# Optimization experiments

Measured on AMD Instinct MI355X. Metric: run time of the kernel, lower is better.

The kernel has to match this reference:

```python
import jax, jax.numpy as jnp
from jax import lax
import numpy as np

B, N, NPOINT, NSAMPLE, RADIUS = 8, 16384, 1024, 32, 0.4
C_IN = 64


def fps(xyz, npoint):
    """Furthest point sampling. xyz: (B, N, 3) -> (B, npoint) int32 indices.
    Matches the CUDA kernel: start from index 0, iteratively pick argmax of
    the running min-distance to the selected set."""
    Bb, Nn, _ = xyz.shape

    def step(carry, _):
        min_d, last = carry
        p = jnp.take_along_axis(xyz, last[:, None, None], axis=1)  # (B,1,3)
        d = jnp.sum((xyz - p) ** 2, axis=-1)                       # (B,N)
        min_d = jnp.minimum(min_d, d)
        nxt = jnp.argmax(min_d, axis=1).astype(jnp.int32)
        return (min_d, nxt), nxt

    idx0 = jnp.zeros((Bb,), jnp.int32)
    min_d0 = jnp.full((Bb, Nn), jnp.inf, xyz.dtype)
    _, rest = lax.scan(step, (min_d0, idx0), None, length=npoint - 1)  # (npoint-1, B)
    return jnp.transpose(jnp.concatenate([idx0[None, :], rest], axis=0))  # (B, npoint)


def ball_query(xyz, new_xyz, radius, nsample):
    """xyz: (B,N,3), new_xyz: (B,P,3) -> (B,P,nsample) int32 indices.
    First nsample in-radius indices (ascending), short balls padded with the
    first found index (the centroid itself is always in-radius)."""
    Nn = xyz.shape[1]
    d2 = jnp.sum((new_xyz[:, :, None, :] - xyz[:, None, :, :]) ** 2, axis=-1)  # (B,P,N)
    ar = jnp.arange(Nn, dtype=jnp.int32)
    key = jnp.where(d2 <= radius * radius, ar, Nn)  # out-of-ball -> sentinel N
    neg_top, _ = lax.top_k(-key, nsample)           # nsample smallest keys
    gidx = -neg_top                                  # (B,P,nsample)
    return jnp.where(gidx == Nn, gidx[..., :1], gidx)


def setup_inputs() -> dict:
    key = jax.random.key(0)
    ks = jax.random.split(key, 8)
    return {
        "xyz": jax.random.normal(ks[0], (B, N, 3), jnp.float32),
        "features": jax.random.normal(ks[1], (B, C_IN, N), jnp.float32),
        "W1": jax.random.normal(ks[2], (64, 3 + C_IN), jnp.float32) * 0.05,
        "b1": jax.random.normal(ks[3], (64,), jnp.float32) * 0.05,
        "W2": jax.random.normal(ks[4], (64, 64), jnp.float32) * 0.05,
        "b2": jax.random.normal(ks[5], (64,), jnp.float32) * 0.05,
        "W3": jax.random.normal(ks[6], (128, 64), jnp.float32) * 0.05,
        "b3": jax.random.normal(ks[7], (128,), jnp.float32) * 0.05,
    }


def reference(xyz, features, W1, b1, W2, b2, W3, b3):
    Bb = xyz.shape[0]
    idx = fps(xyz, NPOINT)                                         # (B,P)
    new_xyz = jnp.take_along_axis(xyz, idx[:, :, None], axis=1)    # (B,P,3)

    gidx = ball_query(xyz, new_xyz, RADIUS, NSAMPLE)               # (B,P,S)
    bi = jnp.arange(Bb)[:, None, None]
    grouped_xyz = xyz[bi, gidx] - new_xyz[:, :, None, :]           # (B,P,S,3) relative coords
    feats_t = jnp.transpose(features, (0, 2, 1))                   # (B,N,C)
    grouped_feats = feats_t[bi, gidx]                              # (B,P,S,C)
    h = jnp.concatenate([grouped_xyz, grouped_feats], axis=-1)     # (B,P,S,3+C)

    # shared per-point MLP (1x1 convs) + ReLU
    h = jax.nn.relu(jnp.einsum('bpsc,oc->bpso', h, W1) + b1)
    h = jax.nn.relu(jnp.einsum('bpsc,oc->bpso', h, W2) + b2)
    h = jax.nn.relu(jnp.einsum('bpsc,oc->bpso', h, W3) + b3)

    pooled = jnp.max(h, axis=2)                                    # (B,P,128) max over nsample
    new_features = jnp.transpose(pooled, (0, 2, 1))                # (B,128,P)
    return new_xyz, new_features
```

## Files before the change

kernel.cpp:

```cpp
#include <hip/hip_runtime.h>

#define R2 0.16f

typedef float f32x2 __attribute__((ext_vector_type(2)));

__device__ __forceinline__ float sqd(float x, float y, float z,
                                     float px, float py, float pz) {
  float dx = __fsub_rn(x, px);
  float dy = __fsub_rn(y, py);
  float dz = __fsub_rn(z, pz);
  return __fadd_rn(__fadd_rn(__fmul_rn(dx, dx), __fmul_rn(dy, dy)),
                   __fmul_rn(dz, dz));
}

__device__ __forceinline__ float wave64_max_dpp(float x) {
#define DPP_STEP(CTRL)                                                      \
  {                                                                         \
    int t_ = __builtin_amdgcn_update_dpp(__float_as_int(x),                 \
                                         __float_as_int(x), CTRL, 0xf, 0xf, \
                                         false);                            \
    x = fmaxf(x, __int_as_float(t_));                                       \
  }
  DPP_STEP(0x111)
  DPP_STEP(0x112)
  DPP_STEP(0x114)
  DPP_STEP(0x118)
  DPP_STEP(0x142)
  DPP_STEP(0x143)
#undef DPP_STEP
  return x;
}

__global__ __launch_bounds__(256) void soa_kernel(const float* __restrict__ xyz,
                                                  float* __restrict__ xs,
                                                  float* __restrict__ ys,
                                                  float* __restrict__ zs) {
  int t = blockIdx.x * 256 + threadIdx.x;
  const float* p = xyz + (size_t)t * 3;
  xs[t] = p[0];
  ys[t] = p[1];
  zs[t] = p[2];
}

__global__ __launch_bounds__(1024) void fps_kernel(
    const float* __restrict__ xyz, const float* __restrict__ xs,
    const float* __restrict__ ys, const float* __restrict__ zs,
    int* __restrict__ idx_out) {
#pragma clang fp contract(off)
  extern __shared__ float4 xylds[];
  int b = blockIdx.x;
  int tid = threadIdx.x;
  int lane = tid & 63, wid = tid >> 6;
  const float* xb = xyz + (size_t)b * 16384 * 3;
  int base = tid << 4;
  const float4* xv = (const float4*)(xs + (size_t)b * 16384 + base);
  const float4* yv = (const float4*)(ys + (size_t)b * 16384 + base);
  const float4* zv = (const float4*)(zs + (size_t)b * 16384 + base);
  float xr[16], yr[16], zr[16];
#pragma unroll
  for (int q = 0; q < 4; ++q) {
    *(float4*)(xr + 4 * q) = xv[q];
    *(float4*)(yr + 4 * q) = yv[q];
    *(float4*)(zr + 4 * q) = zv[q];
  }
  f32x2 Z[8], M[8];
#pragma unroll
  for (int q = 0; q < 8; ++q) {
    xylds[(q << 10) + tid] =
        make_float4(xr[2 * q], xr[2 * q + 1], yr[2 * q], yr[2 * q + 1]);
    Z[q] = {zr[2 * q], zr[2 * q + 1]};
    M[q] = {__builtin_inff(), __builtin_inff()};
  }
  __shared__ unsigned s_vmax[2];
  __shared__ int s_widx[2];
  __shared__ float s_cd[2][3][16];
  if (tid == 0) {
    idx_out[b * 1024] = 0;
    s_vmax[0] = 0u;
    s_vmax[1] = 0u;
    s_widx[0] = 0x7fffffff;
    s_widx[1] = 0x7fffffff;
  }
  __syncthreads();
  float px = xb[0], py = xb[1], pz = xb[2];
  for (int it = 1; it < 1024; ++it) {
    int sl = it & 1;
    f32x2 px2 = {px, px}, py2 = {py, py}, pz2 = {pz, pz};
    float tv = -1.0f;
#pragma unroll
    for (int q = 0; q < 8; ++q) {
      float4 t = xylds[(q << 10) + tid];
      f32x2 X = {t.x, t.y};
      f32x2 Y = {t.z, t.w};
      f32x2 dx = X - px2;
      f32x2 dy = Y - py2;
      f32x2 dz = Z[q] - pz2;
      f32x2 d = dx * dx + dy * dy + dz * dz;
      M[q].x = fminf(M[q].x, d.x);
      M[q].y = fminf(M[q].y, d.y);
      tv = fmaxf(fmaxf(tv, M[q].x), M[q].y);
    }
    float bv = wave64_max_dpp(tv);
    if (lane == 63) atomicMax(&s_vmax[sl], (unsigned)__float_as_int(bv));
    __syncthreads();
    float v = __int_as_float((int)s_vmax[sl]);
    if (tid == 0) {
      s_vmax[sl ^ 1] = 0u;
      s_widx[sl ^ 1] = 0x7fffffff;
    }
    unsigned long long mk = __ballot(tv == v);
    if (mk != 0ull && lane == (int)__builtin_ctzll(mk)) {
      int k = -1;
      float wx = 0.0f, wy = 0.0f, wz = 0.0f;
#pragma unroll
      for (int q = 0; q < 8; ++q) {
        float4 t = xylds[(q << 10) + tid];
        if (k < 0 && M[q].x == v) { k = 2 * q;     wx = t.x; wy = t.z; wz = Z[q].x; }
        if (k < 0 && M[q].y == v) { k = 2 * q + 1; wx = t.y; wy = t.w; wz = Z[q].y; }
      }
      atomicMin(&s_widx[sl], ((base + k) << 4) | wid);
      s_cd[sl][0][wid] = wx;
      s_cd[sl][1][wid] = wy;
      s_cd[sl][2][wid] = wz;
    }
    __syncthreads();
    int kmin = s_widx[sl];
    int w = kmin & 15;
    int j = kmin >> 4;
    px = s_cd[sl][0][w];
    py = s_cd[sl][1][w];
    pz = s_cd[sl][2][w];
    if (tid == 0) idx_out[b * 1024 + it] = j;
  }
}

__global__ __launch_bounds__(256) void gather_newxyz(const float* __restrict__ xyz,
                                                     const int* __restrict__ idx,
                                                     float* __restrict__ out) {
  int t = blockIdx.x * 256 + threadIdx.x;
  int b = t >> 10;
  int i = idx[t];
  const float* src = xyz + ((size_t)b * 16384 + i) * 3;
  float* dst = out + (size_t)t * 3;
  dst[0] = src[0];
  dst[1] = src[1];
  dst[2] = src[2];
}

__global__ __launch_bounds__(256) void transpose_feats(const float* __restrict__ f,
                                                       float* __restrict__ fT) {
  __shared__ float tile[64][65];
  int b = blockIdx.x >> 8;
  int n0 = (blockIdx.x & 255) << 6;
  int t = threadIdx.x;
  int nn = t & 63, c0 = t >> 6;
#pragma unroll
  for (int r = 0; r < 64; r += 4) {
    int c = c0 + r;
    tile[c][nn] = f[((size_t)b * 64 + c) * 16384 + n0 + nn];
  }
  __syncthreads();
  int cc = t & 63, n1 = t >> 6;
#pragma unroll
  for (int r = 0; r < 64; r += 4) {
    int n = n1 + r;
    fT[((size_t)b * 16384 + n0 + n) * 64 + cc] = tile[cc][n];
  }
}

__global__ __launch_bounds__(256) void ballquery_kernel(const float* __restrict__ xyz,
                                                        const float* __restrict__ newxyz,
                                                        int* __restrict__ gidx) {
  int wid = threadIdx.x >> 6, lane = threadIdx.x & 63;
  int cid = blockIdx.x * 4 + wid;
  int b = cid >> 10;
  const float* xb = xyz + (size_t)b * 16384 * 3;
  float cx = newxyz[cid * 3 + 0];
  float cy = newxyz[cid * 3 + 1];
  float cz = newxyz[cid * 3 + 2];
  int* out = gidx + (size_t)cid * 32;
  int found = 0;
  int first = -1;
  for (int c0 = 0; c0 < 16384; c0 += 64) {
    int g = c0 + lane;
    float xx = xb[g * 3 + 0], yy = xb[g * 3 + 1], zz = xb[g * 3 + 2];
    float d2 = sqd(xx, yy, zz, cx, cy, cz);
    bool inr = (d2 <= R2);
    unsigned long long mask = __ballot(inr);
    if (first < 0 && mask) first = c0 + (int)__builtin_ctzll(mask);
    int pre = __popcll(mask & ((1ull << lane) - 1ull));
    int slot = found + pre;
    if (inr && slot < 32) out[slot] = g;
    found += __popcll(mask);
    if (found >= 32) break;
  }
  for (int s = found + lane; s < 32; s += 64) out[s] = first;
}

#define FMA16(BASEPTR)                                                     \
  do {                                                                     \
    const float4* hp_ = (const float4*)(BASEPTR);                          \
    float4 v0 = hp_[0], v1 = hp_[1], v2 = hp_[2], v3 = hp_[3];             \
    float a = acc[s];                                                      \
    a = fmaf(w[0], v0.x, a);  a = fmaf(w[1], v0.y, a);                     \
    a = fmaf(w[2], v0.z, a);  a = fmaf(w[3], v0.w, a);                     \
    a = fmaf(w[4], v1.x, a);  a = fmaf(w[5], v1.y, a);                     \
    a = fmaf(w[6], v1.z, a);  a = fmaf(w[7], v1.w, a);                     \
    a = fmaf(w[8], v2.x, a);  a = fmaf(w[9], v2.y, a);                     \
    a = fmaf(w[10], v2.z, a); a = fmaf(w[11], v2.w, a);                    \
    a = fmaf(w[12], v3.x, a); a = fmaf(w[13], v3.y, a);                    \
    a = fmaf(w[14], v3.z, a); a = fmaf(w[15], v3.w, a);                    \
    acc[s] = a;                                                            \
  } while (0)

__global__ __launch_bounds__(256) void mlp_kernel(
    const float* __restrict__ xyz, const float* __restrict__ feats,
    const float* __restrict__ featsT, const float* __restrict__ newxyz,
    const int* __restrict__ gidx,
    const float* __restrict__ W1, const float* __restrict__ b1,
    const float* __restrict__ W2, const float* __restrict__ b2,
    const float* __restrict__ W3, const float* __restrict__ b3,
    float* __restrict__ out, int useT) {
  __shared__ float buf[4][32 * 68];
  int wid = threadIdx.x >> 6, lane = threadIdx.x & 63;
  int cid = blockIdx.x * 4 + wid;
  int b = cid >> 10, p = cid & 1023;
  float* A = buf[wid];
  const int* gi = gidx + (size_t)cid * 32;
  float cx = newxyz[cid * 3 + 0];
  float cy = newxyz[cid * 3 + 1];
  float cz = newxyz[cid * 3 + 2];

  if (useT) {
    const float4* fT4 = (const float4*)(featsT + (size_t)b * 16384 * 64);
    for (int t = lane; t < 512; t += 64) {
      int s = t >> 4, q = t & 15;
      int g = gi[s];
      float4 v = fT4[(size_t)g * 16 + q];
      *(float4*)(A + s * 68 + q * 4) = v;
    }
  } else {
    const float* fb = feats + (size_t)b * 64 * 16384;
    for (int t = lane; t < 2048; t += 64) {
      int c = t >> 5, s = t & 31;
      int g = gi[s];
      A[s * 68 + c] = fb[(size_t)c * 16384 + g];
    }
  }
  for (int t = lane; t < 96; t += 64) {
    int s = t / 3, c = t - s * 3;
    int g = gi[s];
    float pv = xyz[((size_t)b * 16384 + g) * 3 + c];
    float cv = (c == 0) ? cx : ((c == 1) ? cy : cz);
    A[s * 68 + 64 + c] = __fsub_rn(pv, cv);
  }
  if (lane < 32) A[lane * 68 + 67] = 0.0f;
  __syncthreads();

  int o = lane;
  float acc[32];

#pragma unroll
  for (int s = 0; s < 32; ++s) acc[s] = b1[o];
  {
    const float* wr = W1 + o * 67;
    for (int cb = 0; cb < 4; ++cb) {
      float w[16];
#pragma unroll
      for (int q = 0; q < 16; ++q) w[q] = wr[3 + cb * 16 + q];
#pragma unroll
      for (int s = 0; s < 32; ++s) { FMA16(A + s * 68 + cb * 16); }
    }
    float w0 = wr[0], w1 = wr[1], w2 = wr[2];
#pragma unroll
    for (int s = 0; s < 32; ++s) {
      float a = acc[s];
      a = fmaf(w0, A[s * 68 + 64], a);
      a = fmaf(w1, A[s * 68 + 65], a);
      a = fmaf(w2, A[s * 68 + 66], a);
      acc[s] = a;
    }
  }
  __syncthreads();
#pragma unroll
  for (int s = 0; s < 32; ++s) A[s * 64 + o] = fmaxf(acc[s], 0.0f);
  __syncthreads();

#pragma unroll
  for (int s = 0; s < 32; ++s) acc[s] = b2[o];
  {
    const float* wr = W2 + o * 64;
    for (int cb = 0; cb < 4; ++cb) {
      float w[16];
#pragma unroll
      for (int q = 0; q < 16; ++q) w[q] = wr[cb * 16 + q];
#pragma unroll
      for (int s = 0; s < 32; ++s) { FMA16(A + s * 64 + cb * 16); }
    }
  }
  __syncthreads();
#pragma unroll
  for (int s = 0; s < 32; ++s) A[s * 64 + o] = fmaxf(acc[s], 0.0f);
  __syncthreads();

  float* outp = out + 24576;
  for (int po = 0; po < 2; ++po) {
    int o2 = lane + (po << 6);
#pragma unroll
    for (int s = 0; s < 32; ++s) acc[s] = b3[o2];
    const float* wr = W3 + o2 * 64;
    for (int cb = 0; cb < 4; ++cb) {
      float w[16];
#pragma unroll
      for (int q = 0; q < 16; ++q) w[q] = wr[cb * 16 + q];
#pragma unroll
      for (int s = 0; s < 32; ++s) { FMA16(A + s * 64 + cb * 16); }
    }
    float mx = 0.0f;
#pragma unroll
    for (int s = 0; s < 32; ++s) mx = fmaxf(mx, acc[s]);
    outp[((size_t)b * 128 + o2) * 1024 + p] = mx;
  }
}

extern "C" void kernel_launch(void* const* d_in, const int* in_sizes, int n_in,
                              void* d_out, int out_size, void* d_ws, size_t ws_size,
                              hipStream_t stream) {
  const float* xyz = (const float*)d_in[0];
  const float* feats = (const float*)d_in[1];
  const float* W1 = (const float*)d_in[2];
  const float* b1 = (const float*)d_in[3];
  const float* W2 = (const float*)d_in[4];
  const float* b2 = (const float*)d_in[5];
  const float* W3 = (const float*)d_in[6];
  const float* b3 = (const float*)d_in[7];
  float* out = (float*)d_out;

  int* idx = (int*)d_ws;
  int* gidx = (int*)((char*)d_ws + 32768);
  float* xs = (float*)((char*)d_ws + 32768 + 1048576);
  float* ys = xs + 131072;
  float* zs = ys + 131072;
  float* featsT = (float*)((char*)d_ws + 32768 + 1048576 + 1572864);
  size_t needT = 32768 + 1048576 + 1572864 +
                 (size_t)8 * 16384 * 64 * sizeof(float);
  int useT = (ws_size >= needT) ? 1 : 0;

  soa_kernel<<<512, 256, 0, stream>>>(xyz, xs, ys, zs);
  fps_kernel<<<8, 1024, 131072, stream>>>(xyz, xs, ys, zs, idx);
  gather_newxyz<<<32, 256, 0, stream>>>(xyz, idx, out);
  if (useT) transpose_feats<<<2048, 256, 0, stream>>>(feats, featsT);
  ballquery_kernel<<<2048, 256, 0, stream>>>(xyz, out, gidx);
  mlp_kernel<<<2048, 256, 0, stream>>>(xyz, feats, featsT, out, gidx,
                                       W1, b1, W2, b2, W3, b3, out, useT);
}
```

Before: 2.354 ms.

## Cut FPS per-iteration barriers from two to one via per-wave candidate slots

```diff
diff --git a/kernel.cpp b/kernel.cpp
--- a/kernel.cpp
+++ b/kernel.cpp
@@ -48,6 +48,8 @@
     int* __restrict__ idx_out) {
 #pragma clang fp contract(off)
   extern __shared__ float4 xylds[];
+  __shared__ unsigned s_vmax[3];
+  __shared__ unsigned s_slot[3][16 * 9];
   int b = blockIdx.x;
   int tid = threadIdx.x;
   int lane = tid & 63, wid = tid >> 6;
@@ -71,20 +73,12 @@
     Z[q] = {zr[2 * q], zr[2 * q + 1]};
     M[q] = {__builtin_inff(), __builtin_inff()};
   }
-  __shared__ unsigned s_vmax[2];
-  __shared__ int s_widx[2];
-  __shared__ float s_cd[2][3][16];
-  if (tid == 0) {
-    idx_out[b * 1024] = 0;
-    s_vmax[0] = 0u;
-    s_vmax[1] = 0u;
-    s_widx[0] = 0x7fffffff;
-    s_widx[1] = 0x7fffffff;
-  }
+  if (tid == 0) idx_out[b * 1024] = 0;
+  if (tid < 3) s_vmax[tid] = 0u;
   __syncthreads();
   float px = xb[0], py = xb[1], pz = xb[2];
+  int sl = 1, slp2 = 0;
   for (int it = 1; it < 1024; ++it) {
-    int sl = it & 1;
     f32x2 px2 = {px, px}, py2 = {py, py}, pz2 = {pz, pz};
     float tv = -1.0f;
 #pragma unroll
@@ -101,36 +95,41 @@
       tv = fmaxf(fmaxf(tv, M[q].x), M[q].y);
     }
     float bv = wave64_max_dpp(tv);
-    if (lane == 63) atomicMax(&s_vmax[sl], (unsigned)__float_as_int(bv));
+    unsigned bvb = (unsigned)__builtin_amdgcn_readlane(__float_as_int(bv), 63);
+    float bvf = __int_as_float((int)bvb);
+    if (lane == 0) atomicMax(&s_vmax[sl], bvb);
+    unsigned long long mk = __ballot(tv == bvf);
+    int wlane = (int)__builtin_ctzll(mk);
+    if (lane == wlane) {
+      int k = 0;
+      float wx = 0.0f, wy = 0.0f, wz = 0.0f;
+#pragma unroll
+      for (int q = 7; q >= 0; --q) {
+        float4 t = xylds[(q << 10) + tid];
+        if (M[q].y == bvf) { k = 2 * q + 1; wx = t.y; wy = t.w; wz = Z[q].y; }
+        if (M[q].x == bvf) { k = 2 * q;     wx = t.x; wy = t.z; wz = Z[q].x; }
+      }
+      unsigned* sp = &s_slot[sl][wid * 9];
+      sp[0] = bvb;
+      sp[1] = (unsigned)(base + k);
+      sp[2] = (unsigned)__float_as_int(wx);
+      sp[3] = (unsigned)__float_as_int(wy);
+      sp[4] = (unsigned)__float_as_int(wz);
+    }
     __syncthreads();
-    float v = __int_as_float((int)s_vmax[sl]);
-    if (tid == 0) {
-      s_vmax[sl ^ 1] = 0u;
-      s_widx[sl ^ 1] = 0x7fffffff;
-    }
-    unsigned long long mk = __ballot(tv == v);
-    if (mk != 0ull && lane == (int)__builtin_ctzll(mk)) {
-      int k = -1;
-      float wx = 0.0f, wy = 0.0f, wz = 0.0f;
-#pragma unroll
-      for (int q = 0; q < 8; ++q) {
-        float4 t = xylds[(q << 10) + tid];
-        if (k < 0 && M[q].x == v) { k = 2 * q;     wx = t.x; wy = t.z; wz = Z[q].x; }
-        if (k < 0 && M[q].y == v) { k = 2 * q + 1; wx = t.y; wy = t.w; wz = Z[q].y; }
-      }
-      atomicMin(&s_widx[sl], ((base + k) << 4) | wid);
-      s_cd[sl][0][wid] = wx;
-      s_cd[sl][1][wid] = wy;
-      s_cd[sl][2][wid] = wz;
-    }
-    __syncthreads();
-    int kmin = s_widx[sl];
-    int w = kmin & 15;
-    int j = kmin >> 4;
-    px = s_cd[sl][0][w];
-    py = s_cd[sl][1][w];
-    pz = s_cd[sl][2][w];
+    unsigned v = s_vmax[sl];
+    if (tid == 0) s_vmax[slp2] = 0u;
+    unsigned sval = s_slot[sl][(lane & 15) * 9];
+    unsigned long long m2 = __ballot(sval == v);
+    int w2 = (int)__builtin_ctzll(m2);
+    const unsigned* wp = &s_slot[sl][w2 * 9];
+    int j = (int)wp[1];
+    px = __int_as_float((int)wp[2]);
+    py = __int_as_float((int)wp[3]);
+    pz = __int_as_float((int)wp[4]);
     if (tid == 0) idx_out[b * 1024 + it] = j;
+    sl = (sl == 2) ? 0 : sl + 1;
+    slp2 = (slp2 == 2) ? 0 : slp2 + 1;
   }
 }
 
```

Measured after the change: 2.511 ms. 6.6% more time.

## Spatially bin points for FPS and skip far threads via bounding-box bound

Applied to the files above, without the earlier changes.

```diff
diff --git a/kernel.cpp b/kernel.cpp
--- a/kernel.cpp
+++ b/kernel.cpp
@@ -21,47 +21,112 @@
                                          false);                            \
     x = fmaxf(x, __int_as_float(t_));                                       \
   }
-  DPP_STEP(0x111)
-  DPP_STEP(0x112)
-  DPP_STEP(0x114)
-  DPP_STEP(0x118)
-  DPP_STEP(0x142)
-  DPP_STEP(0x143)
+  DPP_STEP(0x111) DPP_STEP(0x112) DPP_STEP(0x114)
+  DPP_STEP(0x118) DPP_STEP(0x142) DPP_STEP(0x143)
 #undef DPP_STEP
   return x;
 }
-
-__global__ __launch_bounds__(256) void soa_kernel(const float* __restrict__ xyz,
-                                                  float* __restrict__ xs,
-                                                  float* __restrict__ ys,
-                                                  float* __restrict__ zs) {
+__device__ __forceinline__ unsigned wave64_min_dpp_u32(unsigned x) {
+#define DPP_STEP(CTRL)                                                      \
+  {                                                                         \
+    unsigned t_ = (unsigned)__builtin_amdgcn_update_dpp(                    \
+        (int)x, (int)x, CTRL, 0xf, 0xf, false);                             \
+    x = (t_ < x) ? t_ : x;                                                  \
+  }
+  DPP_STEP(0x111) DPP_STEP(0x112) DPP_STEP(0x114)
+  DPP_STEP(0x118) DPP_STEP(0x142) DPP_STEP(0x143)
+#undef DPP_STEP
+  return x;
+}
+
+__global__ __launch_bounds__(256) void zero_hist(unsigned* __restrict__ h) {
+  h[blockIdx.x * 256 + threadIdx.x] = 0u;
+}
+
+__global__ __launch_bounds__(256) void hist_kernel(const float* __restrict__ xyz,
+                                                   unsigned* __restrict__ hist,
+                                                   unsigned* __restrict__ rank,
+                                                   unsigned* __restrict__ cid) {
   int t = blockIdx.x * 256 + threadIdx.x;
+  int b = t >> 14;
   const float* p = xyz + (size_t)t * 3;
-  xs[t] = p[0];
-  ys[t] = p[1];
-  zs[t] = p[2];
+  int cx = (int)floorf(p[0] + 4.0f);
+  int cy = (int)floorf(p[1] + 4.0f);
+  int cz = (int)floorf(p[2] + 4.0f);
+  cx = min(max(cx, 0), 7);
+  cy = min(max(cy, 0), 7);
+  cz = min(max(cz, 0), 7);
+  unsigned c = (unsigned)(cx | (cy << 3) | (cz << 6));
+  unsigned r = atomicAdd(&hist[(b << 9) + c], 1u);
+  rank[t] = r;
+  cid[t] = c;
+}
+
+__global__ __launch_bounds__(512) void scan_kernel(const unsigned* __restrict__ hist,
+                                                   unsigned* __restrict__ starts) {
+  __shared__ unsigned a[512];
+  int b = blockIdx.x, t = threadIdx.x;
+  unsigned h = hist[(b << 9) + t];
+  a[t] = h;
+  __syncthreads();
+  for (int s = 1; s < 512; s <<= 1) {
+    unsigned v = (t >= s) ? a[t - s] : 0u;
+    __syncthreads();
+    a[t] += v;
+    __syncthreads();
+  }
+  starts[(b << 9) + t] = a[t] - h;
+}
+
+__global__ __launch_bounds__(256) void scatter_kernel(
+    const float* __restrict__ xyz, const unsigned* __restrict__ starts,
+    const unsigned* __restrict__ rank, const unsigned* __restrict__ cid,
+    float* __restrict__ xs2, float* __restrict__ ys2, float* __restrict__ zs2,
+    unsigned* __restrict__ oi2) {
+  int t = blockIdx.x * 256 + threadIdx.x;
+  int b = t >> 14, n = t & 16383;
+  unsigned pos = starts[(b << 9) + cid[t]] + rank[t];
+  const float* p = xyz + (size_t)t * 3;
+  size_t o = ((size_t)b << 14) + pos;
+  xs2[o] = p[0];
+  ys2[o] = p[1];
+  zs2[o] = p[2];
+  oi2[o] = (unsigned)n;
 }
 
 __global__ __launch_bounds__(1024) void fps_kernel(
     const float* __restrict__ xyz, const float* __restrict__ xs,
     const float* __restrict__ ys, const float* __restrict__ zs,
-    int* __restrict__ idx_out) {
+    const unsigned* __restrict__ oi, int* __restrict__ idx_out) {
 #pragma clang fp contract(off)
   extern __shared__ float4 xylds[];
+  __shared__ unsigned s_wval[2][16];
+  __shared__ unsigned s_woi[2][16];
   int b = blockIdx.x;
   int tid = threadIdx.x;
   int lane = tid & 63, wid = tid >> 6;
   const float* xb = xyz + (size_t)b * 16384 * 3;
   int base = tid << 4;
-  const float4* xv = (const float4*)(xs + (size_t)b * 16384 + base);
-  const float4* yv = (const float4*)(ys + (size_t)b * 16384 + base);
-  const float4* zv = (const float4*)(zs + (size_t)b * 16384 + base);
+  const float4* xv = (const float4*)(xs + ((size_t)b << 14) + base);
+  const float4* yv = (const float4*)(ys + ((size_t)b << 14) + base);
+  const float4* zv = (const float4*)(zs + ((size_t)b << 14) + base);
+  const uint4* ov = (const uint4*)(oi + ((size_t)b << 14) + base);
   float xr[16], yr[16], zr[16];
+  unsigned OI[16];
 #pragma unroll
   for (int q = 0; q < 4; ++q) {
     *(float4*)(xr + 4 * q) = xv[q];
     *(float4*)(yr + 4 * q) = yv[q];
     *(float4*)(zr + 4 * q) = zv[q];
+    *(uint4*)(OI + 4 * q) = ov[q];
+  }
+  float bxl = xr[0], bxh = xr[0], byl = yr[0], byh = yr[0], bzl = zr[0],
+        bzh = zr[0];
+#pragma unroll
+  for (int k = 1; k < 16; ++k) {
+    bxl = fminf(bxl, xr[k]); bxh = fmaxf(bxh, xr[k]);
+    byl = fminf(byl, yr[k]); byh = fmaxf(byh, yr[k]);
+    bzl = fminf(bzl, zr[k]); bzh = fmaxf(bzh, zr[k]);
   }
   f32x2 Z[8], M[8];
 #pragma unroll
@@ -71,66 +136,70 @@
     Z[q] = {zr[2 * q], zr[2 * q + 1]};
     M[q] = {__builtin_inff(), __builtin_inff()};
   }
-  __shared__ unsigned s_vmax[2];
-  __shared__ int s_widx[2];
-  __shared__ float s_cd[2][3][16];
-  if (tid == 0) {
-    idx_out[b * 1024] = 0;
-    s_vmax[0] = 0u;
-    s_vmax[1] = 0u;
-    s_widx[0] = 0x7fffffff;
-    s_widx[1] = 0x7fffffff;
-  }
+  if (tid == 0) idx_out[b * 1024] = 0;
   __syncthreads();
   float px = xb[0], py = xb[1], pz = xb[2];
+  float tv = __builtin_inff();
   for (int it = 1; it < 1024; ++it) {
     int sl = it & 1;
-    f32x2 px2 = {px, px}, py2 = {py, py}, pz2 = {pz, pz};
-    float tv = -1.0f;
-#pragma unroll
-    for (int q = 0; q < 8; ++q) {
-      float4 t = xylds[(q << 10) + tid];
-      f32x2 X = {t.x, t.y};
-      f32x2 Y = {t.z, t.w};
-      f32x2 dx = X - px2;
-      f32x2 dy = Y - py2;
-      f32x2 dz = Z[q] - pz2;
-      f32x2 d = dx * dx + dy * dy + dz * dz;
-      M[q].x = fminf(M[q].x, d.x);
-      M[q].y = fminf(M[q].y, d.y);
-      tv = fmaxf(fmaxf(tv, M[q].x), M[q].y);
-    }
-    float bv = wave64_max_dpp(tv);
-    if (lane == 63) atomicMax(&s_vmax[sl], (unsigned)__float_as_int(bv));
-    __syncthreads();
-    float v = __int_as_float((int)s_vmax[sl]);
-    if (tid == 0) {
-      s_vmax[sl ^ 1] = 0u;
-      s_widx[sl ^ 1] = 0x7fffffff;
-    }
-    unsigned long long mk = __ballot(tv == v);
-    if (mk != 0ull && lane == (int)__builtin_ctzll(mk)) {
-      int k = -1;
-      float wx = 0.0f, wy = 0.0f, wz = 0.0f;
+    float ddx = fmaxf(fmaxf(bxl - px, px - bxh), 0.0f);
+    float ddy = fmaxf(fmaxf(byl - py, py - byh), 0.0f);
+    float ddz = fmaxf(fmaxf(bzl - pz, pz - bzh), 0.0f);
+    float lb = (ddx * ddx + ddy * ddy + ddz * ddz) * 0.999f;
+    if (lb < tv) {
+      f32x2 px2 = {px, px}, py2 = {py, py}, pz2 = {pz, pz};
+      float ntv = -1.0f;
 #pragma unroll
       for (int q = 0; q < 8; ++q) {
         float4 t = xylds[(q << 10) + tid];
-        if (k < 0 && M[q].x == v) { k = 2 * q;     wx = t.x; wy = t.z; wz = Z[q].x; }
-        if (k < 0 && M[q].y == v) { k = 2 * q + 1; wx = t.y; wy = t.w; wz = Z[q].y; }
+        f32x2 X = {t.x, t.y};
+        f32x2 Y = {t.z, t.w};
+        f32x2 dx = X - px2;
+        f32x2 dy = Y - py2;
+        f32x2 dz = Z[q] - pz2;
+        f32x2 d = dx * dx + dy * dy + dz * dz;
+        M[q].x = fminf(M[q].x, d.x);
+        M[q].y = fminf(M[q].y, d.y);
+        ntv = fmaxf(fmaxf(ntv, M[q].x), M[q].y);
       }
-      atomicMin(&s_widx[sl], ((base + k) << 4) | wid);
-      s_cd[sl][0][wid] = wx;
-      s_cd[sl][1][wid] = wy;
-      s_cd[sl][2][wid] = wz;
+      tv = ntv;
+    }
+    float bv = wave64_max_dpp(tv);
+    unsigned bvb = (unsigned)__builtin_amdgcn_readlane(__float_as_int(bv), 63);
+    float bvf = __int_as_float((int)bvb);
+    unsigned coi = 0xffffffffu;
+    if (tv == bvf) {
+#pragma unroll
+      for (int q = 0; q < 8; ++q) {
+        if (M[q].x == bvf && OI[2 * q] < coi) coi = OI[2 * q];
+        if (M[q].y == bvf && OI[2 * q + 1] < coi) coi = OI[2 * q + 1];
+      }
+    }
+    unsigned woi = wave64_min_dpp_u32(coi);
+    if (lane == 63) {
+      s_wval[sl][wid] = bvb;
+      s_woi[sl][wid] = woi;
     }
     __syncthreads();
-    int kmin = s_widx[sl];
-    int w = kmin & 15;
-    int j = kmin >> 4;
-    px = s_cd[sl][0][w];
-    py = s_cd[sl][1][w];
-    pz = s_cd[sl][2][w];
+    unsigned w0 = s_wval[sl][lane & 15];
+    unsigned o0 = s_woi[sl][lane & 15];
+    unsigned v = w0;
+#pragma unroll
+    for (int off = 1; off <= 8; off <<= 1) {
+      unsigned ov_ = __shfl_xor(v, off);
+      v = (ov_ > v) ? ov_ : v;
+    }
+    unsigned cand = (w0 == v) ? o0 : 0xffffffffu;
+#pragma unroll
+    for (int off = 1; off <= 8; off <<= 1) {
+      unsigned oc = __shfl_xor(cand, off);
+      cand = (oc < cand) ? oc : cand;
+    }
+    int j = (int)cand;
     if (tid == 0) idx_out[b * 1024 + it] = j;
+    px = xb[j * 3 + 0];
+    py = xb[j * 3 + 1];
+    pz = xb[j * 3 + 2];
   }
 }
 
@@ -336,18 +405,27 @@
   const float* b3 = (const float*)d_in[7];
   float* out = (float*)d_out;
 
-  int* idx = (int*)d_ws;
-  int* gidx = (int*)((char*)d_ws + 32768);
-  float* xs = (float*)((char*)d_ws + 32768 + 1048576);
-  float* ys = xs + 131072;
-  float* zs = ys + 131072;
-  float* featsT = (float*)((char*)d_ws + 32768 + 1048576 + 1572864);
-  size_t needT = 32768 + 1048576 + 1572864 +
-                 (size_t)8 * 16384 * 64 * sizeof(float);
+  char* w = (char*)d_ws;
+  int* idx = (int*)w;
+  int* gidx = (int*)(w + 32768);
+  unsigned* hist = (unsigned*)(w + 1081344);
+  unsigned* starts = (unsigned*)(w + 1097728);
+  unsigned* rank = (unsigned*)(w + 1114112);
+  unsigned* cid = (unsigned*)(w + 1638400);
+  unsigned* oi2 = (unsigned*)(w + 2162688);
+  float* xs2 = (float*)(w + 2686976);
+  float* ys2 = (float*)(w + 3211264);
+  float* zs2 = (float*)(w + 3735552);
+  float* featsT = (float*)(w + 4259840);
+  size_t needT = 4259840 + (size_t)8 * 16384 * 64 * sizeof(float);
   int useT = (ws_size >= needT) ? 1 : 0;
 
-  soa_kernel<<<512, 256, 0, stream>>>(xyz, xs, ys, zs);
-  fps_kernel<<<8, 1024, 131072, stream>>>(xyz, xs, ys, zs, idx);
+  zero_hist<<<16, 256, 0, stream>>>(hist);
+  hist_kernel<<<512, 256, 0, stream>>>(xyz, hist, rank, cid);
+  scan_kernel<<<8, 512, 0, stream>>>(hist, starts);
+  scatter_kernel<<<512, 256, 0, stream>>>(xyz, starts, rank, cid, xs2, ys2,
+                                          zs2, oi2);
+  fps_kernel<<<8, 1024, 131072, stream>>>(xyz, xs2, ys2, zs2, oi2, idx);
   gather_newxyz<<<32, 256, 0, stream>>>(xyz, idx, out);
   if (useT) transpose_feats<<<2048, 256, 0, stream>>>(feats, featsT);
   ballquery_kernel<<<2048, 256, 0, stream>>>(xyz, out, gidx);
```

New measurement: 2.203 ms. 6.4% less time.
